# Kernel optimization log

Measured on AMD Instinct MI355X. Metric: run time of the kernel, lower is better.

The kernel has to match this reference:

```python
import jax, jax.numpy as jnp
import numpy as np

# ---- static config (matches init_kwargs) ----
B, L, D, H, NC = 2, 4096, 256, 8, 3
TOP_N, R = 8, 32              # top_n, vicinity_radius
LS, LE = 1000, 3000           # label_start, label_end
NL = 2                        # n_cross_attn_layers
FF = 4 * D                    # ffn_expand * d_model
Q_MAX = 2 * TOP_N * (2 * R + 1)  # 1040
HD = D // H


def setup_inputs() -> dict:
    key = jax.random.key(0)
    ks = jax.random.split(key, 12)
    def rn(k, shape, s=0.05):
        return jax.random.normal(k, shape, jnp.float32) * s
    return {
        "encoder_output": jax.random.normal(ks[0], (B, L, D), jnp.float32),
        "coarse_logits": jax.random.normal(ks[1], (B, L, NC), jnp.float32),
        "ln_q_g": jnp.ones((NL, D), jnp.float32),
        "ln_q_b": jnp.zeros((NL, D), jnp.float32),
        "ln_kv_g": jnp.ones((NL, D), jnp.float32),
        "ln_kv_b": jnp.zeros((NL, D), jnp.float32),
        "Wq": rn(ks[2], (NL, D, D)), "bq": jnp.zeros((NL, D), jnp.float32),
        "Wk": rn(ks[3], (NL, D, D)), "bk": jnp.zeros((NL, D), jnp.float32),
        "Wv": rn(ks[4], (NL, D, D)), "bv": jnp.zeros((NL, D), jnp.float32),
        "Wo": rn(ks[5], (NL, D, D)), "bo": jnp.zeros((NL, D), jnp.float32),
        "ffn_g": jnp.ones((NL, D), jnp.float32),
        "ffn_b": jnp.zeros((NL, D), jnp.float32),
        "W1": rn(ks[6], (NL, D, FF)), "b1": jnp.zeros((NL, FF), jnp.float32),
        "W2": rn(ks[7], (NL, FF, D)), "b2": jnp.zeros((NL, D), jnp.float32),
        "head_W": rn(ks[8], (D, NC)), "head_b": jnp.zeros((NC,), jnp.float32),
    }


def _layer_norm(x, g, b, eps=1e-5):
    m = jnp.mean(x, axis=-1, keepdims=True)
    v = jnp.mean(jnp.square(x - m), axis=-1, keepdims=True)
    return (x - m) * jax.lax.rsqrt(v + eps) * g + b


def _select_vicinities(coarse_logits):
    # eval mode: no gumbel noise. Returns (vicinity_idx (B,Q_MAX) int32 with
    # sentinel L at pad/dup slots, q_pad_mask (B,Q_MAX) bool).
    lp = jax.nn.log_softmax(coarse_logits.astype(jnp.float32), axis=-1)
    pos = jnp.arange(L)
    region = (pos >= LS) & (pos < LE)
    acc = jnp.where(region, lp[..., 1], -jnp.inf)
    don = jnp.where(region, lp[..., 2], -jnp.inf)
    _, don_idx = jax.lax.top_k(don, TOP_N)
    _, acc_idx = jax.lax.top_k(acc, TOP_N)
    centers = jnp.concatenate([don_idx, acc_idx], axis=-1)        # (B, 2*TOP_N)
    offsets = jnp.arange(-R, R + 1)
    vic = jnp.clip(centers[:, :, None] + offsets, 0, L - 1).reshape(B, -1)
    s = jnp.sort(vic, axis=-1)
    is_first = jnp.concatenate(
        [jnp.ones((B, 1), bool), s[:, 1:] != s[:, :-1]], axis=-1)
    idx = jnp.where(is_first, s, L)  # sentinel L -> zero row of scratch
    return idx, is_first


def reference(encoder_output, coarse_logits, ln_q_g, ln_q_b, ln_kv_g, ln_kv_b,
              Wq, bq, Wk, bk, Wv, bv, Wo, bo, ffn_g, ffn_b, W1, b1, W2, b2,
              head_W, head_b):
    idx, mask = _select_vicinities(coarse_logits)      # torch.no_grad() region
    idx = jax.lax.stop_gradient(idx)
    mask = jax.lax.stop_gradient(mask)

    scratch = jnp.pad(encoder_output, ((0, 0), (0, 1), (0, 0)))   # (B, L+1, D)
    q_stream = jnp.take_along_axis(scratch, idx[:, :, None], axis=1)  # (B,Q,D)
    kv = encoder_output
    m3 = mask[:, :, None]

    for i in range(NL):
        q_in = _layer_norm(q_stream, ln_q_g[i], ln_q_b[i])
        kv_in = _layer_norm(kv, ln_kv_g[i], ln_kv_b[i])
        q = (q_in @ Wq[i] + bq[i]).reshape(B, Q_MAX, H, HD)
        k = (kv_in @ Wk[i] + bk[i]).reshape(B, L, H, HD)
        v = (kv_in @ Wv[i] + bv[i]).reshape(B, L, H, HD)
        scores = jnp.einsum('bqhd,bkhd->bhqk', q, k) / jnp.sqrt(
            jnp.float32(HD))
        attn = jax.nn.softmax(scores, axis=-1)
        ao = jnp.einsum('bhqk,bkhd->bqhd', attn, v).reshape(B, Q_MAX, D)
        q_stream = q_stream + ao @ Wo[i] + bo[i]
        q_stream = jnp.where(m3, q_stream, 0.0)
        h = _layer_norm(q_stream, ffn_g[i], ffn_b[i])
        h = jax.nn.gelu(h @ W1[i] + b1[i], approximate=False) @ W2[i] + b2[i]
        q_stream = jnp.where(m3, q_stream + h, 0.0)

    out_scratch = scratch.at[jnp.arange(B)[:, None], idx].set(q_stream)
    refined = out_scratch[:, :L]                                  # drop sentinel
    refined_logits = refined @ head_W + head_b                    # (B, L, 3)
    return refined_logits
```

## Files before the change

### kernel.cpp

```cpp
#include <hip/hip_runtime.h>
#include <cmath>

constexpr int B = 2, L = 4096, D = 256, H = 8, NC = 3;
constexpr int TOP_N = 8, R = 32;
constexpr int LS = 1000, LE = 3000;
constexpr int NL = 2;
constexpr int FF = 4 * D;
constexpr int Q_MAX = 2 * TOP_N * (2 * R + 1);
constexpr int HD = D / H;
constexpr int QROWS = B * Q_MAX;
constexpr int KVROWS = B * L;
constexpr int NQT = (Q_MAX + 31) / 32;
constexpr int NREG = LE - LS;
constexpr int NSPLIT = 8;
constexpr int KCHUNK = L / NSPLIT;
constexpr int NT = KCHUNK / 32;
constexpr int KVBLK = 8 * (KVROWS / 64);
constexpr int QBLK = 4 * ((QROWS + 63) / 64);

typedef __attribute__((ext_vector_type(8))) short bf16x8;
typedef __attribute__((ext_vector_type(4))) float f32x4;
typedef __attribute__((ext_vector_type(4))) int i32x4;
typedef unsigned short u16;

union fr {
  bf16x8 h;
  i32x4 i;
};

__device__ __forceinline__ u16 f2bs(float f) {
  unsigned int u = __float_as_uint(f);
  unsigned int r = u + 0x7fffu + ((u >> 16) & 1u);
  return (u16)(r >> 16);
}
__device__ __forceinline__ float bs2f(u16 s) {
  return __uint_as_float(((unsigned int)s) << 16);
}
__device__ __forceinline__ float gelu_exact(float x) {
  return 0.5f * x * (1.f + erff(x * 0.70710678118654752440f));
}
__device__ __forceinline__ unsigned cvt_pk(float lo, float hi) {
  unsigned r;
  asm("v_cvt_pk_bf16_f32 %0, %1, %2" : "=v"(r) : "v"(lo), "v"(hi));
  return r;
}

#define GLL16(gsrc, ldst)                                                   \
  __builtin_amdgcn_global_load_lds(                                         \
      (const __attribute__((address_space(1))) unsigned int*)(gsrc),        \
      (__attribute__((address_space(3))) unsigned int*)(ldst), 16, 0, 0)

__global__ __launch_bounds__(1024) void select_kernel(
    const float* __restrict__ logits, int* __restrict__ idx_out,
    int* __restrict__ mask_out) {
  int b = blockIdx.x;
  int tid = threadIdx.x;
  int w = tid >> 6, lane = tid & 63;
  __shared__ float candv[16][8];
  __shared__ int candi[16][8];
  __shared__ int centers[2 * TOP_N];
  __shared__ unsigned present[L / 32];
  __shared__ int offs[128];
  __shared__ int wtot[2];

  float vd[2], va[2];
  int pidx[2];
#pragma unroll
  for (int j = 0; j < 2; ++j) {
    int p = tid + j * 1024;
    pidx[j] = p;
    if (p < NREG) {
      const float* lg = logits + ((long)b * L + LS + p) * NC;
      float x0 = lg[0], x1 = lg[1], x2 = lg[2];
      float m = fmaxf(x0, fmaxf(x1, x2));
      float lse = m + logf(expf(x0 - m) + expf(x1 - m) + expf(x2 - m));
      vd[j] = x2 - lse;
      va[j] = x1 - lse;
    } else {
      vd[j] = -INFINITY;
      va[j] = -INFINITY;
    }
  }
  if (tid < 128) present[tid] = 0;

  for (int sel = 0; sel < 2; ++sel) {
    float v0 = (sel == 0) ? vd[0] : va[0];
    float v1 = (sel == 0) ? vd[1] : va[1];
#pragma unroll
    for (int r = 0; r < TOP_N; ++r) {
      float mv;
      int mi;
      if (v0 >= v1) { mv = v0; mi = pidx[0]; }
      else { mv = v1; mi = pidx[1]; }
#pragma unroll
      for (int off = 32; off; off >>= 1) {
        float ov = __shfl_xor(mv, off, 64);
        int oi = __shfl_xor(mi, off, 64);
        if (ov > mv || (ov == mv && oi < mi)) { mv = ov; mi = oi; }
      }
      if (pidx[0] == mi) v0 = -INFINITY;
      if (pidx[1] == mi) v1 = -INFINITY;
      if (lane == 0) { candv[w][r] = mv; candi[w][r] = mi; }
    }
    __syncthreads();
    if (tid < 64) {
      int j0 = tid, j1 = tid + 64;
      float c0 = candv[j0 >> 3][j0 & 7], c1 = candv[j1 >> 3][j1 & 7];
      int i0 = candi[j0 >> 3][j0 & 7], i1 = candi[j1 >> 3][j1 & 7];
#pragma unroll
      for (int r = 0; r < TOP_N; ++r) {
        float mv;
        int mi;
        if (c0 > c1 || (c0 == c1 && i0 < i1)) { mv = c0; mi = i0; }
        else { mv = c1; mi = i1; }
#pragma unroll
        for (int off = 32; off; off >>= 1) {
          float ov = __shfl_xor(mv, off, 64);
          int oi = __shfl_xor(mi, off, 64);
          if (ov > mv || (ov == mv && oi < mi)) { mv = ov; mi = oi; }
        }
        if (i0 == mi) c0 = -INFINITY;
        if (i1 == mi) c1 = -INFINITY;
        if (tid == 0) centers[sel * TOP_N + r] = LS + mi;
      }
    }
    __syncthreads();
  }

  for (int j = tid; j < Q_MAX; j += 1024) {
    int c = centers[j / (2 * R + 1)];
    int off = j % (2 * R + 1) - R;
    int v = c + off;
    v = v < 0 ? 0 : (v > L - 1 ? L - 1 : v);
    atomicOr(&present[v >> 5], 1u << (v & 31));
  }
  __syncthreads();

  int cnt = (tid < 128) ? __popc(present[tid]) : 0;
  if (tid < 128) {
    int x = cnt;
#pragma unroll
    for (int off = 1; off < 64; off <<= 1) {
      int o = __shfl_up(x, off, 64);
      if ((tid & 63) >= off) x += o;
    }
    if ((tid & 63) == 63) wtot[tid >> 6] = x;
    offs[tid] = x - cnt;
  }
  __syncthreads();
  int total = wtot[0] + wtot[1];
  if (tid < 128) {
    int base = offs[tid] + ((tid >= 64) ? wtot[0] : 0);
    unsigned mword = present[tid];
    while (mword) {
      int i = __ffs(mword) - 1;
      mword &= mword - 1;
      idx_out[b * Q_MAX + base] = tid * 32 + i;
      mask_out[b * Q_MAX + base] = 1;
      ++base;
    }
  }
  for (int j = total + tid; j < Q_MAX; j += 1024) {
    idx_out[b * Q_MAX + j] = L;
    mask_out[b * Q_MAX + j] = 0;
  }
}

__global__ __launch_bounds__(256) void gather_kernel(
    const float* __restrict__ enc, const int* __restrict__ idx,
    float* __restrict__ q_stream) {
  int row = blockIdx.x;
  int b = row / Q_MAX;
  int p = idx[row];
  float v = 0.f;
  if (p < L) v = enc[((long)b * L + p) * D + threadIdx.x];
  q_stream[(long)row * D + threadIdx.x] = v;
}

__global__ __launch_bounds__(256) void ln_bf16(
    const float* __restrict__ in, u16* __restrict__ out,
    const float* __restrict__ gg, const float* __restrict__ bb) {
  long row = blockIdx.x;
  int tid = threadIdx.x;
  float x = in[row * D + tid];
  float s1 = x, s2 = x * x;
#pragma unroll
  for (int off = 32; off; off >>= 1) {
    s1 += __shfl_xor(s1, off, 64);
    s2 += __shfl_xor(s2, off, 64);
  }
  __shared__ float p1[4], p2[4];
  int w = tid >> 6;
  if ((tid & 63) == 0) { p1[w] = s1; p2[w] = s2; }
  __syncthreads();
  s1 = p1[0] + p1[1] + p1[2] + p1[3];
  s2 = p2[0] + p2[1] + p2[2] + p2[3];
  float mean = s1 * (1.f / D);
  float var = fmaxf(s2 * (1.f / D) - mean * mean, 0.f);
  float r = rsqrtf(var + 1e-5f);
  out[row * D + tid] = f2bs((x - mean) * r * gg[tid] + bb[tid]);
}

__global__ __launch_bounds__(256) void ln_kv2(
    const float* __restrict__ in, u16* __restrict__ o0, u16* __restrict__ o1,
    const float* __restrict__ gg, const float* __restrict__ bb) {
  long row = blockIdx.x;
  int tid = threadIdx.x;
  float x = in[row * D + tid];
  float s1 = x, s2 = x * x;
#pragma unroll
  for (int off = 32; off; off >>= 1) {
    s1 += __shfl_xor(s1, off, 64);
    s2 += __shfl_xor(s2, off, 64);
  }
  __shared__ float p1[4], p2[4];
  int w = tid >> 6;
  if ((tid & 63) == 0) { p1[w] = s1; p2[w] = s2; }
  __syncthreads();
  s1 = p1[0] + p1[1] + p1[2] + p1[3];
  s2 = p2[0] + p2[1] + p2[2] + p2[3];
  float mean = s1 * (1.f / D);
  float var = fmaxf(s2 * (1.f / D) - mean * mean, 0.f);
  float r = rsqrtf(var + 1e-5f);
  float xn = (x - mean) * r;
  o0[row * D + tid] = f2bs(xn * gg[tid] + bb[tid]);
  o1[row * D + tid] = f2bs(xn * gg[D + tid] + bb[D + tid]);
}

__global__ __launch_bounds__(256) void transpose_tiled(
    const float* __restrict__ Wq_, const float* __restrict__ Wk_,
    const float* __restrict__ Wv_, const float* __restrict__ Wo_,
    const float* __restrict__ W1_, const float* __restrict__ W2_,
    u16* __restrict__ WT) {
  __shared__ u16 T[64][65];
  const long DD = (long)D * D, DFF = (long)D * FF;
  const long LSTR = 4 * DD + 2 * DFF;
  int t = blockIdx.x;
  int l = t / 192, r = t % 192;
  const float* src;
  long dbase;
  int K_, N_, kt, nt;
  if (r < 64) {
    int which = r >> 4, sub = r & 15;
    kt = sub >> 2;
    nt = sub & 3;
    K_ = 256;
    N_ = 256;
    src = (which == 0 ? Wk_ : which == 1 ? Wv_ : which == 2 ? Wq_ : Wo_) +
          (long)l * DD;
    dbase = (long)l * LSTR + (long)which * DD;
  } else if (r < 128) {
    int sub = r - 64;
    kt = sub >> 4;
    nt = sub & 15;
    K_ = 256;
    N_ = 1024;
    src = W1_ + (long)l * DFF;
    dbase = (long)l * LSTR + 4 * DD;
  } else {
    int sub = r - 128;
    kt = sub >> 2;
    nt = sub & 3;
    K_ = 1024;
    N_ = 256;
    src = W2_ + (long)l * DFF;
    dbase = (long)l * LSTR + 4 * DD + DFF;
  }
  int k0 = kt * 64, n0 = nt * 64;
  {
    int kr = threadIdx.x >> 2, c16 = (threadIdx.x & 3) * 16;
    const float* sp = src + (long)(k0 + kr) * N_ + n0 + c16;
#pragma unroll
    for (int i = 0; i < 4; ++i) {
      float4 v = *reinterpret_cast<const float4*>(sp + 4 * i);
      T[kr][c16 + 4 * i + 0] = f2bs(v.x);
      T[kr][c16 + 4 * i + 1] = f2bs(v.y);
      T[kr][c16 + 4 * i + 2] = f2bs(v.z);
      T[kr][c16 + 4 * i + 3] = f2bs(v.w);
    }
  }
  __syncthreads();
  {
    int nr = threadIdx.x >> 2, kc = (threadIdx.x & 3) * 16;
    u16 tmp[16];
#pragma unroll
    for (int j = 0; j < 16; ++j) tmp[j] = T[kc + j][nr];
    u16* dp = WT + dbase + (long)(n0 + nr) * K_ + k0 + kc;
    *reinterpret_cast<bf16x8*>(dp) = *reinterpret_cast<const bf16x8*>(&tmp[0]);
    *reinterpret_cast<bf16x8*>(dp + 8) =
        *reinterpret_cast<const bf16x8*>(&tmp[8]);
  }
}

template <int EPI>
__global__ __launch_bounds__(256) void gemm_mfma(
    const u16* __restrict__ A, const u16* __restrict__ BT,
    const float* __restrict__ bias, void* __restrict__ Cv,
    const float* __restrict__ resid, const int* __restrict__ mask, int M,
    int N, int K) {
  __shared__ short As[64][40];
  __shared__ short Bs[64][40];
  int bm = blockIdx.y * 64, bn = blockIdx.x * 64;
  int tid = threadIdx.x;
  int lane = tid & 63, w = tid >> 6;
  int g = lane >> 4, li = lane & 15;
  int wr = w >> 1, wc = w & 1;
  f32x4 acc[2][2] = {};

  int srow = tid >> 2, skc = (tid & 3) * 8;
  for (int k0 = 0; k0 < K; k0 += 32) {
    {
      int grow = bm + srow;
      bf16x8 av = {};
      if (grow < M)
        av = *reinterpret_cast<const bf16x8*>(A + (long)grow * K + k0 + skc);
      *reinterpret_cast<bf16x8*>(&As[srow][skc]) = av;
      bf16x8 bv = *reinterpret_cast<const bf16x8*>(
          BT + (long)(bn + srow) * K + k0 + skc);
      *reinterpret_cast<bf16x8*>(&Bs[srow][skc]) = bv;
    }
    __syncthreads();
    bf16x8 a0 = *reinterpret_cast<const bf16x8*>(&As[wr * 32 + li][g * 8]);
    bf16x8 a1 = *reinterpret_cast<const bf16x8*>(&As[wr * 32 + 16 + li][g * 8]);
    bf16x8 b0 = *reinterpret_cast<const bf16x8*>(&Bs[wc * 32 + li][g * 8]);
    bf16x8 b1 = *reinterpret_cast<const bf16x8*>(&Bs[wc * 32 + 16 + li][g * 8]);
    acc[0][0] = __builtin_amdgcn_mfma_f32_16x16x32_bf16(a0, b0, acc[0][0], 0, 0, 0);
    acc[0][1] = __builtin_amdgcn_mfma_f32_16x16x32_bf16(a0, b1, acc[0][1], 0, 0, 0);
    acc[1][0] = __builtin_amdgcn_mfma_f32_16x16x32_bf16(a1, b0, acc[1][0], 0, 0, 0);
    acc[1][1] = __builtin_amdgcn_mfma_f32_16x16x32_bf16(a1, b1, acc[1][1], 0, 0, 0);
    __syncthreads();
  }

#pragma unroll
  for (int mr = 0; mr < 2; ++mr)
#pragma unroll
    for (int nr = 0; nr < 2; ++nr)
#pragma unroll
      for (int r = 0; r < 4; ++r) {
        int row = bm + wr * 32 + mr * 16 + g * 4 + r;
        int col = bn + wc * 32 + nr * 16 + li;
        if (row >= M) continue;
        float v = acc[mr][nr][r] + bias[col];
        if (EPI == 1) v = gelu_exact(v);
        if (EPI == 2) {
          v += resid[(long)row * N + col];
          v = mask[row] ? v : 0.f;
          ((float*)Cv)[(long)row * N + col] = v;
        } else {
          ((u16*)Cv)[(long)row * N + col] = f2bs(v);
        }
      }
}

__global__ __launch_bounds__(256) void gemm_proj(
    const u16* __restrict__ Akv, const u16* __restrict__ Aq,
    const u16* __restrict__ WTbase, const float* __restrict__ biasK,
    const float* __restrict__ biasV, const float* __restrict__ biasQ,
    u16* __restrict__ Kh, u16* __restrict__ Vh, u16* __restrict__ Qb) {
  __shared__ short As[64][40];
  __shared__ short Bs[64][40];
  __shared__ u16 Ct[64][72];
  int bid = blockIdx.x;
  int tid = threadIdx.x;
  int lane = tid & 63, w = tid >> 6;
  int g = lane >> 4, li = lane & 15;
  int wr = w >> 1, wc = w & 1;
  f32x4 acc[2][2] = {};
  const long DD = (long)D * D;

  bool isKV = bid < KVBLK;
  int bm, bn, M;
  const u16* A;
  const u16* BT;
  if (isKV) {
    bn = (bid & 7) * 64;
    bm = (bid >> 3) * 64;
    M = KVROWS;
    A = Akv;
    BT = WTbase;
  } else {
    int qb = bid - KVBLK;
    bn = (qb & 3) * 64;
    bm = (qb >> 2) * 64;
    M = QROWS;
    A = Aq;
    BT = WTbase + 2 * DD;
  }

  int srow = tid >> 2, skc = (tid & 3) * 8;
  for (int k0 = 0; k0 < D; k0 += 32) {
    {
      int grow = bm + srow;
      bf16x8 av = {};
      if (grow < M)
        av = *reinterpret_cast<const bf16x8*>(A + (long)grow * D + k0 + skc);
      *reinterpret_cast<bf16x8*>(&As[srow][skc]) = av;
      bf16x8 bv = *reinterpret_cast<const bf16x8*>(
          BT + (long)(bn + srow) * D + k0 + skc);
      *reinterpret_cast<bf16x8*>(&Bs[srow][skc]) = bv;
    }
    __syncthreads();
    bf16x8 a0 = *reinterpret_cast<const bf16x8*>(&As[wr * 32 + li][g * 8]);
    bf16x8 a1 = *reinterpret_cast<const bf16x8*>(&As[wr * 32 + 16 + li][g * 8]);
    bf16x8 b0 = *reinterpret_cast<const bf16x8*>(&Bs[wc * 32 + li][g * 8]);
    bf16x8 b1 = *reinterpret_cast<const bf16x8*>(&Bs[wc * 32 + 16 + li][g * 8]);
    acc[0][0] = __builtin_amdgcn_mfma_f32_16x16x32_bf16(a0, b0, acc[0][0], 0, 0, 0);
    acc[0][1] = __builtin_amdgcn_mfma_f32_16x16x32_bf16(a0, b1, acc[0][1], 0, 0, 0);
    acc[1][0] = __builtin_amdgcn_mfma_f32_16x16x32_bf16(a1, b0, acc[1][0], 0, 0, 0);
    acc[1][1] = __builtin_amdgcn_mfma_f32_16x16x32_bf16(a1, b1, acc[1][1], 0, 0, 0);
    __syncthreads();
  }

  if (!isKV) {
#pragma unroll
    for (int mr = 0; mr < 2; ++mr)
#pragma unroll
      for (int nr = 0; nr < 2; ++nr)
#pragma unroll
        for (int r = 0; r < 4; ++r) {
          int row = bm + wr * 32 + mr * 16 + g * 4 + r;
          int col = bn + wc * 32 + nr * 16 + li;
          if (row >= M) continue;
          Qb[(long)row * D + col] = f2bs(acc[mr][nr][r] + biasQ[col]);
        }
  } else if (bn < 256) {
#pragma unroll
    for (int mr = 0; mr < 2; ++mr)
#pragma unroll
      for (int nr = 0; nr < 2; ++nr)
#pragma unroll
        for (int r = 0; r < 4; ++r) {
          int rowL = wr * 32 + mr * 16 + g * 4 + r;
          int colL = wc * 32 + nr * 16 + li;
          Ct[rowL][colL] = f2bs(acc[mr][nr][r] + biasK[bn + colL]);
        }
    __syncthreads();
#pragma unroll
    for (int p = 0; p < 2; ++p) {
      int rowL = (tid >> 3) + p * 32;
      int c8 = (tid & 7) * 8;
      int grow = bm + rowL;
      int b2 = grow >> 12, key = grow & (L - 1);
      int gcol = bn + c8;
      int hh = gcol >> 5, dd = gcol & (HD - 1);
      int cst = (dd >> 3) ^ ((key >> 1) & 3);
      u16* dst = Kh + (((long)(b2 * H + hh) * L + key) * 32 + (cst << 3));
      *reinterpret_cast<bf16x8*>(dst) =
          *reinterpret_cast<const bf16x8*>(&Ct[rowL][c8]);
    }
  } else {
    int vbn = bn - 256;
#pragma unroll
    for (int mr = 0; mr < 2; ++mr)
#pragma unroll
      for (int nr = 0; nr < 2; ++nr)
#pragma unroll
        for (int r = 0; r < 4; ++r) {
          int rowL = wr * 32 + mr * 16 + g * 4 + r;
          int colL = wc * 32 + nr * 16 + li;
          Ct[colL][rowL] = f2bs(acc[mr][nr][r] + biasV[vbn + colL]);
        }
    __syncthreads();
    int b2 = bm >> 12;
#pragma unroll
    for (int p = 0; p < 2; ++p) {
      int colL = (tid >> 3) + p * 32;
      int rem = tid & 7;
      int kb = rem >> 2, k8 = (rem & 3) * 8;
      int gcol = vbn + colL;
      int hh = gcol >> 5, dd = gcol & (HD - 1);
      int kb32 = ((bm & (L - 1)) >> 5) + kb;
      int j = (k8 >> 2) ^ ((dd >> 1) & 6);
      u16* dst = Vh + (((long)(b2 * H + hh) * (L / 32) + kb32) * 1024 +
                       dd * 32 + (j << 2));
      *reinterpret_cast<bf16x8*>(dst) =
          *reinterpret_cast<const bf16x8*>(&Ct[colL][kb * 32 + k8]);
    }
  }
}

constexpr int POOLSZ = NSPLIT * 32 * 33 * 4 + NSPLIT * 32 * 4;

__global__ __launch_bounds__(512) void attn_mfma(
    const u16* __restrict__ Qb, const u16* __restrict__ Kh,
    const u16* __restrict__ Vh, u16* __restrict__ AO) {
  __shared__ alignas(16) char pool[POOLSZ];
  int i = blockIdx.x;
  int xcd = i & 7, slot = i >> 3;
  int bh = (xcd << 1) | (slot >= NQT ? 1 : 0);
  int qt = (slot >= NQT) ? slot - NQT : slot;
  int h = bh & 7;
  int b = bh >> 3;
  int tid = threadIdx.x, w = tid >> 6, lane = tid & 63;
  int g = lane >> 4, li = lane & 15;

  fr qf0, qf1;
  {
    const float QSC = 0.25509836048f;
#pragma unroll
    for (int qb = 0; qb < 2; ++qb) {
      int qrow = qt * 32 + qb * 16 + li;
      if (qrow >= Q_MAX) qrow = Q_MAX - 1;
      bf16x8 raw = *reinterpret_cast<const bf16x8*>(
          Qb + ((long)(b * Q_MAX + qrow)) * D + h * HD + g * 8);
      fr& qf = qb ? qf1 : qf0;
#pragma unroll
      for (int j = 0; j < 4; ++j)
        qf.i[j] = (int)cvt_pk(bs2f((u16)raw[2 * j]) * QSC,
                              bs2f((u16)raw[2 * j + 1]) * QSC);
    }
  }

  f32x4 acc00 = {}, acc01 = {}, acc10 = {}, acc11 = {};
// ... 47 lines not shown
    for (int r = 0; r < 4; ++r) {
      p00[r] = exp2f(s00[r]);
      p10[r] = exp2f(s10[r]);
      p01[r] = exp2f(s01[r]);
      p11[r] = exp2f(s11[r]);
      den0 += p00[r] + p10[r];
      den1 += p01[r] + p11[r];
    }
    fr pf0, pf1;
    pf0.i[0] = (int)cvt_pk(p00[0], p00[1]);
    pf0.i[1] = (int)cvt_pk(p00[2], p00[3]);
    pf0.i[2] = (int)cvt_pk(p10[0], p10[1]);
    pf0.i[3] = (int)cvt_pk(p10[2], p10[3]);
    pf1.i[0] = (int)cvt_pk(p01[0], p01[1]);
    pf1.i[1] = (int)cvt_pk(p01[2], p01[3]);
    pf1.i[2] = (int)cvt_pk(p11[0], p11[1]);
    pf1.i[3] = (int)cvt_pk(p11[2], p11[3]);

    fr v0, v1;
    v0.i = (i32x4){(int)va0.x, (int)va0.y, (int)vb0.x, (int)vb0.y};
    v1.i = (i32x4){(int)va1.x, (int)va1.y, (int)vb1.x, (int)vb1.y};
    acc00 = __builtin_amdgcn_mfma_f32_16x16x32_bf16(v0.h, pf0.h, acc00, 0, 0, 0);
    acc01 = __builtin_amdgcn_mfma_f32_16x16x32_bf16(v0.h, pf1.h, acc01, 0, 0, 0);
    acc10 = __builtin_amdgcn_mfma_f32_16x16x32_bf16(v1.h, pf0.h, acc10, 0, 0, 0);
    acc11 = __builtin_amdgcn_mfma_f32_16x16x32_bf16(v1.h, pf1.h, acc11, 0, 0, 0);
  }

  den0 += __shfl_xor(den0, 16, 64);
  den0 += __shfl_xor(den0, 32, 64);
  den1 += __shfl_xor(den1, 16, 64);
  den1 += __shfl_xor(den1, 32, 64);

  __syncthreads();
  float (*accs)[32][33] = (float(*)[32][33])pool;
  float (*dsh)[32] = (float(*)[32])(pool + NSPLIT * 32 * 33 * 4);
#pragma unroll
  for (int r = 0; r < 4; ++r) {
    accs[w][g * 4 + r][li] = acc00[r];
    accs[w][g * 4 + r][16 + li] = acc01[r];
    accs[w][16 + g * 4 + r][li] = acc10[r];
    accs[w][16 + g * 4 + r][16 + li] = acc11[r];
  }
  if (g == 0) {
    dsh[w][li] = den0;
    dsh[w][16 + li] = den1;
  }
  __syncthreads();

  int q = tid >> 4, dp = tid & 15;
  float Den = 0.f, o0 = 0.f, o1 = 0.f;
#pragma unroll
  for (int ww = 0; ww < NSPLIT; ++ww) {
    Den += dsh[ww][q];
    o0 += accs[ww][2 * dp][q];
    o1 += accs[ww][2 * dp + 1][q];
  }
  float inv = 1.f / Den;
  int qrow = qt * 32 + q;
  if (qrow < Q_MAX) {
    unsigned pk = cvt_pk(o0 * inv, o1 * inv);
    *reinterpret_cast<unsigned*>(
        AO + ((long)(b * Q_MAX + qrow)) * D + h * HD + 2 * dp) = pk;
  }
}

__global__ __launch_bounds__(256) void head_kernel(
    const float* __restrict__ enc, const float* __restrict__ hW,
    const float* __restrict__ hb, float* __restrict__ out) {
// ... 45 lines not shown
extern "C" void kernel_launch(void* const* d_in, const int* in_sizes, int n_in,
                              void* d_out, int out_size, void* d_ws,
                              size_t ws_size, hipStream_t stream) {
  const float* enc = (const float*)d_in[0];
  const float* clog = (const float*)d_in[1];
  const float* ln_q_g = (const float*)d_in[2];
  const float* ln_q_b = (const float*)d_in[3];
  const float* ln_kv_g = (const float*)d_in[4];
  const float* ln_kv_b = (const float*)d_in[5];
  const float* Wq = (const float*)d_in[6];
  const float* bq = (const float*)d_in[7];
  const float* Wk = (const float*)d_in[8];
  const float* bk = (const float*)d_in[9];
  const float* Wv = (const float*)d_in[10];
  const float* bv = (const float*)d_in[11];
  const float* Wo = (const float*)d_in[12];
  const float* bo = (const float*)d_in[13];
  const float* ffn_g = (const float*)d_in[14];
  const float* ffn_b = (const float*)d_in[15];
  const float* W1 = (const float*)d_in[16];
  const float* b1 = (const float*)d_in[17];
  const float* W2 = (const float*)d_in[18];
  const float* b2 = (const float*)d_in[19];
  const float* head_W = (const float*)d_in[20];
  const float* head_b = (const float*)d_in[21];
  float* out = (float*)d_out;

  char* ws = (char*)d_ws;
  float* q_stream = (float*)ws;            ws += (long)QROWS * D * 4;
  u16* kvl0 = (u16*)ws;                    ws += (long)KVROWS * D * 2;
  u16* kvl1 = (u16*)ws;                    ws += (long)KVROWS * D * 2;
  u16* Khbuf = (u16*)ws;                   ws += (long)B * H * L * HD * 2;
  u16* Vhbuf = (u16*)ws;                   ws += (long)B * H * L * HD * 2;
  u16* q_ln = (u16*)ws;                    ws += (long)QROWS * D * 2;
  u16* Qbuf = (u16*)ws;                    ws += (long)QROWS * D * 2;
  u16* AObuf = (u16*)ws;                   ws += (long)QROWS * D * 2;
  u16* H1buf = (u16*)ws;                   ws += (long)QROWS * FF * 2;
  u16* WT = (u16*)ws;                      ws += (long)NL * (4 * D * D + 2 * D * FF) * 2;
  int* idxbuf = (int*)ws;                  ws += QROWS * 4;
  int* maskbuf = (int*)ws;

  const long DD = (long)D * D, DFF = (long)D * FF;
  const long LSTR = 4 * DD + 2 * DFF;

  transpose_tiled<<<NL * 192, 256, 0, stream>>>(Wq, Wk, Wv, Wo, W1, W2, WT);
  ln_kv2<<<KVROWS, 256, 0, stream>>>(enc, kvl0, kvl1, ln_kv_g, ln_kv_b);
  select_kernel<<<B, 1024, 0, stream>>>(clog, idxbuf, maskbuf);
  gather_kernel<<<QROWS, 256, 0, stream>>>(enc, idxbuf, q_stream);

  for (int l = 0; l < NL; ++l) {
    u16* base = WT + l * LSTR;
    u16* kv_ln = (l == 0) ? kvl0 : kvl1;

    ln_bf16<<<QROWS, 256, 0, stream>>>(q_stream, q_ln, ln_q_g + l * D, ln_q_b + l * D);

    gemm_proj<<<KVBLK + QBLK, 256, 0, stream>>>(
        kv_ln, q_ln, base, bk + l * D, bv + l * D, bq + l * D, Khbuf, Vhbuf,
        Qbuf);

    attn_mfma<<<B * H * NQT, 512, 0, stream>>>(Qbuf, Khbuf, Vhbuf, AObuf);

    dim3 gQ(D / 64, (QROWS + 63) / 64);
    gemm_mfma<2><<<gQ, 256, 0, stream>>>(AObuf, base + 3 * DD, bo + l * D,
                                         (void*)q_stream, q_stream, maskbuf,
                                         QROWS, D, D);

    ln_bf16<<<QROWS, 256, 0, stream>>>(q_stream, q_ln, ffn_g + l * D, ffn_b + l * D);
    dim3 gF1(FF / 64, (QROWS + 63) / 64);
    gemm_mfma<1><<<gF1, 256, 0, stream>>>(q_ln, base + 4 * DD, b1 + l * FF,
                                          (void*)H1buf, nullptr, nullptr,
                                          QROWS, FF, D);
    dim3 gF2(D / 64, (QROWS + 63) / 64);
    gemm_mfma<2><<<gF2, 256, 0, stream>>>(H1buf, base + 4 * DD + DFF,
                                          b2 + l * D, (void*)q_stream,
                                          q_stream, maskbuf, QROWS, D, FF);
  }

  head_kernel<<<KVROWS / 4, 256, 0, stream>>>(enc, head_W, head_b, out);
  overwrite_kernel<<<QROWS, 64, 0, stream>>>(q_stream, idxbuf, maskbuf, head_W,
                                             head_b, out);
}
```

Before: 230.5 us.

## Fuse setup kernels and fold query/FFN layernorms into GEMM prologues

Merges the weight transpose, KV layernorm and vicinity selection into one setup kernel, and reworks selection to use 256 threads. Removes the standalone ln_bf16 launches by computing the layernorm inside the Q projection and FFN1 GEMMs, with a full 64x256 normalized A tile staged in shared memory. This cuts kernel launches and intermediate bf16 round trips. The cost is fewer, longer-running blocks for the Q and FFN1 GEMMs, which may lower parallelism.

```diff
diff --git a/kernel.cpp b/kernel.cpp
--- a/kernel.cpp
+++ b/kernel.cpp
@@ -16,7 +16,8 @@
 constexpr int KCHUNK = L / NSPLIT;
 constexpr int NT = KCHUNK / 32;
 constexpr int KVBLK = 8 * (KVROWS / 64);
-constexpr int QBLK = 4 * ((QROWS + 63) / 64);
+constexpr int QRB = (QROWS + 63) / 64;
+constexpr int TRBLK = NL * 192;
 
 typedef __attribute__((ext_vector_type(8))) short bf16x8;
 typedef __attribute__((ext_vector_type(4))) float f32x4;
@@ -50,119 +51,213 @@
       (const __attribute__((address_space(1))) unsigned int*)(gsrc),        \
       (__attribute__((address_space(3))) unsigned int*)(ldst), 16, 0, 0)
 
-__global__ __launch_bounds__(1024) void select_kernel(
-    const float* __restrict__ logits, int* __restrict__ idx_out,
-    int* __restrict__ mask_out) {
-  int b = blockIdx.x;
+__global__ __launch_bounds__(256) void setup_kernel(
+    const float* __restrict__ enc, const float* __restrict__ logits,
+    const float* __restrict__ lnkvg, const float* __restrict__ lnkvb,
+    const float* __restrict__ Wq_, const float* __restrict__ Wk_,
+    const float* __restrict__ Wv_, const float* __restrict__ Wo_,
+    const float* __restrict__ W1_, const float* __restrict__ W2_,
+    u16* __restrict__ WT, u16* __restrict__ o0, u16* __restrict__ o1,
+    int* __restrict__ idx_out, int* __restrict__ mask_out) {
+  int bid = blockIdx.x;
   int tid = threadIdx.x;
-  int w = tid >> 6, lane = tid & 63;
-  __shared__ float candv[16][8];
-  __shared__ int candi[16][8];
-  __shared__ int centers[2 * TOP_N];
-  __shared__ unsigned present[L / 32];
-  __shared__ int offs[128];
-  __shared__ int wtot[2];
-
-  float vd[2], va[2];
-  int pidx[2];
-#pragma unroll
-  for (int j = 0; j < 2; ++j) {
-    int p = tid + j * 1024;
-    pidx[j] = p;
-    if (p < NREG) {
-      const float* lg = logits + ((long)b * L + LS + p) * NC;
-      float x0 = lg[0], x1 = lg[1], x2 = lg[2];
-      float m = fmaxf(x0, fmaxf(x1, x2));
-      float lse = m + logf(expf(x0 - m) + expf(x1 - m) + expf(x2 - m));
-      vd[j] = x2 - lse;
-      va[j] = x1 - lse;
+  const long DD = (long)D * D, DFF = (long)D * FF;
+  const long LSTR = 4 * DD + 2 * DFF;
+
+  if (bid < KVROWS) {
+    long row = bid;
+    float x = enc[row * D + tid];
+    float s1 = x, s2 = x * x;
+#pragma unroll
+    for (int off = 32; off; off >>= 1) {
+      s1 += __shfl_xor(s1, off, 64);
+      s2 += __shfl_xor(s2, off, 64);
+    }
+    __shared__ float p1[4], p2[4];
+    int w = tid >> 6;
+    if ((tid & 63) == 0) { p1[w] = s1; p2[w] = s2; }
+    __syncthreads();
+    s1 = p1[0] + p1[1] + p1[2] + p1[3];
+    s2 = p2[0] + p2[1] + p2[2] + p2[3];
+    float mean = s1 * (1.f / D);
+    float var = fmaxf(s2 * (1.f / D) - mean * mean, 0.f);
+    float r = rsqrtf(var + 1e-5f);
+    float xn = (x - mean) * r;
+    o0[row * D + tid] = f2bs(xn * lnkvg[tid] + lnkvb[tid]);
+    o1[row * D + tid] = f2bs(xn * lnkvg[D + tid] + lnkvb[D + tid]);
+    return;
+  }
+
+  if (bid < KVROWS + TRBLK) {
+    __shared__ u16 T[64][65];
+    int t = bid - KVROWS;
+    int l = t / 192, r = t % 192;
+    const float* src;
+    long dbase;
+    int K_, N_, kt, nt;
+    if (r < 64) {
+      int which = r >> 4, sub = r & 15;
+      kt = sub >> 2;
+      nt = sub & 3;
+      K_ = 256;
+      N_ = 256;
+      src = (which == 0 ? Wk_ : which == 1 ? Wv_ : which == 2 ? Wq_ : Wo_) +
+            (long)l * DD;
+      dbase = (long)l * LSTR + (long)which * DD;
+    } else if (r < 128) {
+      int sub = r - 64;
+      kt = sub >> 4;
+      nt = sub & 15;
+      K_ = 256;
+      N_ = 1024;
+      src = W1_ + (long)l * DFF;
+      dbase = (long)l * LSTR + 4 * DD;
     } else {
-      vd[j] = -INFINITY;
-      va[j] = -INFINITY;
-    }
-  }
-  if (tid < 128) present[tid] = 0;
-
-  for (int sel = 0; sel < 2; ++sel) {
-    float v0 = (sel == 0) ? vd[0] : va[0];
-    float v1 = (sel == 0) ? vd[1] : va[1];
-#pragma unroll
-    for (int r = 0; r < TOP_N; ++r) {
-      float mv;
-      int mi;
-      if (v0 >= v1) { mv = v0; mi = pidx[0]; }
-      else { mv = v1; mi = pidx[1]; }
-#pragma unroll
-      for (int off = 32; off; off >>= 1) {
-        float ov = __shfl_xor(mv, off, 64);
-        int oi = __shfl_xor(mi, off, 64);
-        if (ov > mv || (ov == mv && oi < mi)) { mv = ov; mi = oi; }
+      int sub = r - 128;
+      kt = sub >> 2;
+      nt = sub & 3;
+      K_ = 1024;
+      N_ = 256;
+      src = W2_ + (long)l * DFF;
+      dbase = (long)l * LSTR + 4 * DD + DFF;
+    }
+    int k0 = kt * 64, n0 = nt * 64;
+    {
+      int kr = tid >> 2, c16 = (tid & 3) * 16;
+      const float* sp = src + (long)(k0 + kr) * N_ + n0 + c16;
+#pragma unroll
+      for (int i = 0; i < 4; ++i) {
+        float4 v = *reinterpret_cast<const float4*>(sp + 4 * i);
+        T[kr][c16 + 4 * i + 0] = f2bs(v.x);
+        T[kr][c16 + 4 * i + 1] = f2bs(v.y);
+        T[kr][c16 + 4 * i + 2] = f2bs(v.z);
+        T[kr][c16 + 4 * i + 3] = f2bs(v.w);
       }
-      if (pidx[0] == mi) v0 = -INFINITY;
-      if (pidx[1] == mi) v1 = -INFINITY;
-      if (lane == 0) { candv[w][r] = mv; candi[w][r] = mi; }
-    }
-    __syncthreads();
-    if (tid < 64) {
-      int j0 = tid, j1 = tid + 64;
-      float c0 = candv[j0 >> 3][j0 & 7], c1 = candv[j1 >> 3][j1 & 7];
-      int i0 = candi[j0 >> 3][j0 & 7], i1 = candi[j1 >> 3][j1 & 7];
+    }
+    __syncthreads();
+    {
+      int nr = tid >> 2, kc = (tid & 3) * 16;
+      u16 tmp[16];
+#pragma unroll
+      for (int j = 0; j < 16; ++j) tmp[j] = T[kc + j][nr];
+      u16* dp = WT + dbase + (long)(n0 + nr) * K_ + k0 + kc;
+      *reinterpret_cast<bf16x8*>(dp) = *reinterpret_cast<const bf16x8*>(&tmp[0]);
+      *reinterpret_cast<bf16x8*>(dp + 8) =
+          *reinterpret_cast<const bf16x8*>(&tmp[8]);
+    }
+    return;
+  }
+
+  {
+    int b = bid - KVROWS - TRBLK;
+    int w = tid >> 6, lane = tid & 63;
+    __shared__ float candv[4][8];
+    __shared__ int candi[4][8];
+    __shared__ int centers[2 * TOP_N];
+    __shared__ unsigned present[L / 32];
+    __shared__ int offs[128];
+    __shared__ int wtot[2];
+
+    float vd[8], va[8];
+#pragma unroll
+    for (int j = 0; j < 8; ++j) {
+      int p = tid + j * 256;
+      if (p < NREG) {
+        const float* lg = logits + ((long)b * L + LS + p) * NC;
+        float x0 = lg[0], x1 = lg[1], x2 = lg[2];
+        float m = fmaxf(x0, fmaxf(x1, x2));
+        float lse = m + logf(expf(x0 - m) + expf(x1 - m) + expf(x2 - m));
+        vd[j] = x2 - lse;
+        va[j] = x1 - lse;
+      } else {
+        vd[j] = -INFINITY;
+        va[j] = -INFINITY;
+      }
+    }
+    if (tid < 128) present[tid] = 0;
+
+    for (int sel = 0; sel < 2; ++sel) {
+      float v[8];
+#pragma unroll
+      for (int j = 0; j < 8; ++j) v[j] = (sel == 0) ? vd[j] : va[j];
 #pragma unroll
       for (int r = 0; r < TOP_N; ++r) {
-        float mv;
-        int mi;
-        if (c0 > c1 || (c0 == c1 && i0 < i1)) { mv = c0; mi = i0; }
-        else { mv = c1; mi = i1; }
+        float mv = v[0];
+        int mp = tid;
+#pragma unroll
+        for (int j = 1; j < 8; ++j) {
+          int pj = tid + j * 256;
+          if (v[j] > mv) { mv = v[j]; mp = pj; }
+        }
 #pragma unroll
         for (int off = 32; off; off >>= 1) {
           float ov = __shfl_xor(mv, off, 64);
-          int oi = __shfl_xor(mi, off, 64);
-          if (ov > mv || (ov == mv && oi < mi)) { mv = ov; mi = oi; }
+          int oi = __shfl_xor(mp, off, 64);
+          if (ov > mv || (ov == mv && oi < mp)) { mv = ov; mp = oi; }
         }
-        if (i0 == mi) c0 = -INFINITY;
-        if (i1 == mi) c1 = -INFINITY;
-        if (tid == 0) centers[sel * TOP_N + r] = LS + mi;
+#pragma unroll
+        for (int j = 0; j < 8; ++j)
+          if (tid + j * 256 == mp) v[j] = -INFINITY;
+        if (lane == 0) { candv[w][r] = mv; candi[w][r] = mp; }
       }
-    }
-    __syncthreads();
-  }
-
-  for (int j = tid; j < Q_MAX; j += 1024) {
-    int c = centers[j / (2 * R + 1)];
-    int off = j % (2 * R + 1) - R;
-    int v = c + off;
-    v = v < 0 ? 0 : (v > L - 1 ? L - 1 : v);
-    atomicOr(&present[v >> 5], 1u << (v & 31));
-  }
-  __syncthreads();
-
-  int cnt = (tid < 128) ? __popc(present[tid]) : 0;
-  if (tid < 128) {
-    int x = cnt;
-#pragma unroll
-    for (int off = 1; off < 64; off <<= 1) {
-      int o = __shfl_up(x, off, 64);
-      if ((tid & 63) >= off) x += o;
-    }
-    if ((tid & 63) == 63) wtot[tid >> 6] = x;
-    offs[tid] = x - cnt;
-  }
-  __syncthreads();
-  int total = wtot[0] + wtot[1];
-  if (tid < 128) {
-    int base = offs[tid] + ((tid >= 64) ? wtot[0] : 0);
-    unsigned mword = present[tid];
-    while (mword) {
-      int i = __ffs(mword) - 1;
-      mword &= mword - 1;
-      idx_out[b * Q_MAX + base] = tid * 32 + i;
-      mask_out[b * Q_MAX + base] = 1;
-      ++base;
-    }
-  }
-  for (int j = total + tid; j < Q_MAX; j += 1024) {
-    idx_out[b * Q_MAX + j] = L;
-    mask_out[b * Q_MAX + j] = 0;
+      __syncthreads();
+      if (tid < 64) {
+        float c = (tid < 32) ? candv[tid >> 3][tid & 7] : -INFINITY;
+        int ci = (tid < 32) ? candi[tid >> 3][tid & 7] : 0x7fffffff;
+#pragma unroll
+        for (int r = 0; r < TOP_N; ++r) {
+          float mv = c;
+          int mi = ci;
+#pragma unroll
+          for (int off = 32; off; off >>= 1) {
+            float ov = __shfl_xor(mv, off, 64);
+            int oi = __shfl_xor(mi, off, 64);
+            if (ov > mv || (ov == mv && oi < mi)) { mv = ov; mi = oi; }
+          }
+          if (ci == mi) c = -INFINITY;
+          if (tid == 0) centers[sel * TOP_N + r] = LS + mi;
+        }
+      }
+      __syncthreads();
+    }
+
+    for (int j = tid; j < Q_MAX; j += 256) {
+      int c = centers[j / (2 * R + 1)];
+      int off = j % (2 * R + 1) - R;
+      int v2 = c + off;
+      v2 = v2 < 0 ? 0 : (v2 > L - 1 ? L - 1 : v2);
+      atomicOr(&present[v2 >> 5], 1u << (v2 & 31));
+    }
+    __syncthreads();
+
+    int cnt = (tid < 128) ? __popc(present[tid]) : 0;
+    if (tid < 128) {
+      int x = cnt;
+#pragma unroll
+      for (int off = 1; off < 64; off <<= 1) {
+        int o = __shfl_up(x, off, 64);
+        if ((tid & 63) >= off) x += o;
+      }
+      if ((tid & 63) == 63) wtot[tid >> 6] = x;
+      offs[tid] = x - cnt;
+    }
+    __syncthreads();
+    int total = wtot[0] + wtot[1];
+    if (tid < 128) {
+      int base = offs[tid] + ((tid >= 64) ? wtot[0] : 0);
+      unsigned mword = present[tid];
+      while (mword) {
+        int i = __ffs(mword) - 1;
+        mword &= mword - 1;
+        idx_out[b * Q_MAX + base] = tid * 32 + i;
+        mask_out[b * Q_MAX + base] = 1;
+        ++base;
+      }
+    }
+    for (int j = total + tid; j < Q_MAX; j += 256) {
+      idx_out[b * Q_MAX + j] = L;
+      mask_out[b * Q_MAX + j] = 0;
+    }
   }
 }
 
@@ -177,118 +272,46 @@
   q_stream[(long)row * D + threadIdx.x] = v;
 }
 
-__global__ __launch_bounds__(256) void ln_bf16(
-    const float* __restrict__ in, u16* __restrict__ out,
-    const float* __restrict__ gg, const float* __restrict__ bb) {
-  long row = blockIdx.x;
-  int tid = threadIdx.x;
-  float x = in[row * D + tid];
-  float s1 = x, s2 = x * x;
-#pragma unroll
-  for (int off = 32; off; off >>= 1) {
-    s1 += __shfl_xor(s1, off, 64);
-    s2 += __shfl_xor(s2, off, 64);
-  }
-  __shared__ float p1[4], p2[4];
-  int w = tid >> 6;
-  if ((tid & 63) == 0) { p1[w] = s1; p2[w] = s2; }
-  __syncthreads();
-  s1 = p1[0] + p1[1] + p1[2] + p1[3];
-  s2 = p2[0] + p2[1] + p2[2] + p2[3];
-  float mean = s1 * (1.f / D);
-  float var = fmaxf(s2 * (1.f / D) - mean * mean, 0.f);
-  float r = rsqrtf(var + 1e-5f);
-  out[row * D + tid] = f2bs((x - mean) * r * gg[tid] + bb[tid]);
-}
-
-__global__ __launch_bounds__(256) void ln_kv2(
-    const float* __restrict__ in, u16* __restrict__ o0, u16* __restrict__ o1,
-    const float* __restrict__ gg, const float* __restrict__ bb) {
-  long row = blockIdx.x;
-  int tid = threadIdx.x;
-  float x = in[row * D + tid];
-  float s1 = x, s2 = x * x;
-#pragma unroll
-  for (int off = 32; off; off >>= 1) {
-    s1 += __shfl_xor(s1, off, 64);
-    s2 += __shfl_xor(s2, off, 64);
-  }
-  __shared__ float p1[4], p2[4];
-  int w = tid >> 6;
-  if ((tid & 63) == 0) { p1[w] = s1; p2[w] = s2; }
-  __syncthreads();
-  s1 = p1[0] + p1[1] + p1[2] + p1[3];
-  s2 = p2[0] + p2[1] + p2[2] + p2[3];
-  float mean = s1 * (1.f / D);
-  float var = fmaxf(s2 * (1.f / D) - mean * mean, 0.f);
-  float r = rsqrtf(var + 1e-5f);
-  float xn = (x - mean) * r;
-  o0[row * D + tid] = f2bs(xn * gg[tid] + bb[tid]);
-  o1[row * D + tid] = f2bs(xn * gg[D + tid] + bb[D + tid]);
-}
-
-__global__ __launch_bounds__(256) void transpose_tiled(
-    const float* __restrict__ Wq_, const float* __restrict__ Wk_,
-    const float* __restrict__ Wv_, const float* __restrict__ Wo_,
-    const float* __restrict__ W1_, const float* __restrict__ W2_,
-    u16* __restrict__ WT) {
-  __shared__ u16 T[64][65];
-  const long DD = (long)D * D, DFF = (long)D * FF;
-  const long LSTR = 4 * DD + 2 * DFF;
-  int t = blockIdx.x;
-  int l = t / 192, r = t % 192;
-  const float* src;
-  long dbase;
-  int K_, N_, kt, nt;
-  if (r < 64) {
-    int which = r >> 4, sub = r & 15;
-    kt = sub >> 2;
-    nt = sub & 3;
-    K_ = 256;
-    N_ = 256;
-    src = (which == 0 ? Wk_ : which == 1 ? Wv_ : which == 2 ? Wq_ : Wo_) +
-          (long)l * DD;
-    dbase = (long)l * LSTR + (long)which * DD;
-  } else if (r < 128) {
-    int sub = r - 64;
-    kt = sub >> 4;
-    nt = sub & 15;
-    K_ = 256;
-    N_ = 1024;
-    src = W1_ + (long)l * DFF;
-    dbase = (long)l * LSTR + 4 * DD;
-  } else {
-    int sub = r - 128;
-    kt = sub >> 2;
-    nt = sub & 3;
-    K_ = 1024;
-    N_ = 256;
-    src = W2_ + (long)l * DFF;
-    dbase = (long)l * LSTR + 4 * DD + DFF;
-  }
-  int k0 = kt * 64, n0 = nt * 64;
-  {
-    int kr = threadIdx.x >> 2, c16 = (threadIdx.x & 3) * 16;
-    const float* sp = src + (long)(k0 + kr) * N_ + n0 + c16;
-#pragma unroll
-    for (int i = 0; i < 4; ++i) {
-      float4 v = *reinterpret_cast<const float4*>(sp + 4 * i);
-      T[kr][c16 + 4 * i + 0] = f2bs(v.x);
-      T[kr][c16 + 4 * i + 1] = f2bs(v.y);
-      T[kr][c16 + 4 * i + 2] = f2bs(v.z);
-      T[kr][c16 + 4 * i + 3] = f2bs(v.w);
-    }
-  }
-  __syncthreads();
-  {
-    int nr = threadIdx.x >> 2, kc = (threadIdx.x & 3) * 16;
-    u16 tmp[16];
-#pragma unroll
-    for (int j = 0; j < 16; ++j) tmp[j] = T[kc + j][nr];
-    u16* dp = WT + dbase + (long)(n0 + nr) * K_ + k0 + kc;
-    *reinterpret_cast<bf16x8*>(dp) = *reinterpret_cast<const bf16x8*>(&tmp[0]);
-    *reinterpret_cast<bf16x8*>(dp + 8) =
-        *reinterpret_cast<const bf16x8*>(&tmp[8]);
+__device__ __forceinline__ void ln_stage(
+    const float* __restrict__ A, int bm, int M, const float* __restrict__ lng,
+    const float* __restrict__ lnb, u16 (*As)[264], int tid) {
+  int r = tid >> 2, qd = tid & 3;
+  int grow = bm + r;
+  if (grow >= M) grow = M - 1;
+  const float* ap = A + ((long)grow) * D + qd * 64;
+  float sum = 0.f, ss = 0.f;
+#pragma unroll
+  for (int i = 0; i < 16; ++i) {
+    float4 v = *reinterpret_cast<const float4*>(ap + i * 4);
+    sum += v.x + v.y + v.z + v.w;
+    ss += v.x * v.x + v.y * v.y + v.z * v.z + v.w * v.w;
+  }
+  sum += __shfl_xor(sum, 1, 64);
+  sum += __shfl_xor(sum, 2, 64);
+  ss += __shfl_xor(ss, 1, 64);
+  ss += __shfl_xor(ss, 2, 64);
+  float mean = sum * (1.f / D);
+  float var = fmaxf(ss * (1.f / D) - mean * mean, 0.f);
+  float rstd = rsqrtf(var + 1e-5f);
+#pragma unroll
+  for (int i = 0; i < 8; ++i) {
+    int k = qd * 64 + i * 8;
+    float4 xa = *reinterpret_cast<const float4*>(ap + i * 8);
+    float4 xb = *reinterpret_cast<const float4*>(ap + i * 8 + 4);
+    float4 ga = *reinterpret_cast<const float4*>(lng + k);
+    float4 gb = *reinterpret_cast<const float4*>(lng + k + 4);
+    float4 ba = *reinterpret_cast<const float4*>(lnb + k);
+    float4 bb = *reinterpret_cast<const float4*>(lnb + k + 4);
+    fr v;
+    v.i[0] = (int)cvt_pk((xa.x - mean) * rstd * ga.x + ba.x,
+                         (xa.y - mean) * rstd * ga.y + ba.y);
+    v.i[1] = (int)cvt_pk((xa.z - mean) * rstd * ga.z + ba.z,
+                         (xa.w - mean) * rstd * ga.w + ba.w);
+    v.i[2] = (int)cvt_pk((xb.x - mean) * rstd * gb.x + bb.x,
+                         (xb.y - mean) * rstd * gb.y + bb.y);
+    v.i[3] = (int)cvt_pk((xb.z - mean) * rstd * gb.z + bb.z,
+                         (xb.w - mean) * rstd * gb.w + bb.w);
+    *reinterpret_cast<bf16x8*>(&As[r][k]) = v.h;
   }
 }
 
@@ -353,50 +376,75 @@
 }
 
 __global__ __launch_bounds__(256) void gemm_proj(
-    const u16* __restrict__ Akv, const u16* __restrict__ Aq,
-    const u16* __restrict__ WTbase, const float* __restrict__ biasK,
+    const u16* __restrict__ Akv, const float* __restrict__ Aqf,
+    const u16* __restrict__ WTbase, const float* __restrict__ lnqg,
+    const float* __restrict__ lnqb, const float* __restrict__ biasK,
     const float* __restrict__ biasV, const float* __restrict__ biasQ,
     u16* __restrict__ Kh, u16* __restrict__ Vh, u16* __restrict__ Qb) {
-  __shared__ short As[64][40];
-  __shared__ short Bs[64][40];
-  __shared__ u16 Ct[64][72];
+  __shared__ alignas(16) char pool[64 * 264 * 2 + 64 * 40 * 2];
   int bid = blockIdx.x;
   int tid = threadIdx.x;
   int lane = tid & 63, w = tid >> 6;
   int g = lane >> 4, li = lane & 15;
   int wr = w >> 1, wc = w & 1;
+  const long DD = (long)D * D;
+
+  if (bid >= KVBLK) {
+    u16(*As)[264] = (u16(*)[264])pool;
+    u16(*Bs)[40] = (u16(*)[40])(pool + 64 * 264 * 2);
+    int bm = (bid - KVBLK) * 64;
+    ln_stage(Aqf, bm, QROWS, lnqg, lnqb, As, tid);
+    __syncthreads();
+    const u16* BT = WTbase + 2 * DD;
+    int srow = tid >> 2, skc = (tid & 3) * 8;
+    for (int nt = 0; nt < 4; ++nt) {
+      int bn = nt * 64;
+      f32x4 acc[2][2] = {};
+      for (int k0 = 0; k0 < D; k0 += 32) {
+        *reinterpret_cast<bf16x8*>(&Bs[srow][skc]) =
+            *reinterpret_cast<const bf16x8*>(BT + (long)(bn + srow) * D + k0 + skc);
+        __syncthreads();
+        bf16x8 a0 = *reinterpret_cast<const bf16x8*>(&As[wr * 32 + li][k0 + g * 8]);
+        bf16x8 a1 =
+            *reinterpret_cast<const bf16x8*>(&As[wr * 32 + 16 + li][k0 + g * 8]);
+        bf16x8 b0 = *reinterpret_cast<const bf16x8*>(&Bs[wc * 32 + li][g * 8]);
+        bf16x8 b1 = *reinterpret_cast<const bf16x8*>(&Bs[wc * 32 + 16 + li][g * 8]);
+        acc[0][0] = __builtin_amdgcn_mfma_f32_16x16x32_bf16(a0, b0, acc[0][0], 0, 0, 0);
+        acc[0][1] = __builtin_amdgcn_mfma_f32_16x16x32_bf16(a0, b1, acc[0][1], 0, 0, 0);
+        acc[1][0] = __builtin_amdgcn_mfma_f32_16x16x32_bf16(a1, b0, acc[1][0], 0, 0, 0);
+        acc[1][1] = __builtin_amdgcn_mfma_f32_16x16x32_bf16(a1, b1, acc[1][1], 0, 0, 0);
+        __syncthreads();
+      }
+#pragma unroll
+      for (int mr = 0; mr < 2; ++mr)
+#pragma unroll
+        for (int nr = 0; nr < 2; ++nr)
+#pragma unroll
+          for (int r = 0; r < 4; ++r) {
+            int row = bm + wr * 32 + mr * 16 + g * 4 + r;
+            int col = bn + wc * 32 + nr * 16 + li;
+            if (row >= QROWS) continue;
+            Qb[(long)row * D + col] = f2bs(acc[mr][nr][r] + biasQ[col]);
+          }
+    }
+    return;
+  }
+
+  short(*As)[40] = (short(*)[40])pool;
+  short(*Bs)[40] = (short(*)[40])(pool + 64 * 40 * 2);
+  u16(*Ct)[72] = (u16(*)[72])(pool + 2 * 64 * 40 * 2);
+  int bn = (bid & 7) * 64;
+  int bm = (bid >> 3) * 64;
   f32x4 acc[2][2] = {};
-  const long DD = (long)D * D;
-
-  bool isKV = bid < KVBLK;
-  int bm, bn, M;
-  const u16* A;
-  const u16* BT;
-  if (isKV) {
-    bn = (bid & 7) * 64;
-    bm = (bid >> 3) * 64;
-    M = KVROWS;
-    A = Akv;
-    BT = WTbase;
-  } else {
-    int qb = bid - KVBLK;
-    bn = (qb & 3) * 64;
-    bm = (qb >> 2) * 64;
-    M = QROWS;
-    A = Aq;
-    BT = WTbase + 2 * DD;
-  }
 
   int srow = tid >> 2, skc = (tid & 3) * 8;
   for (int k0 = 0; k0 < D; k0 += 32) {
     {
-      int grow = bm + srow;
-      bf16x8 av = {};
-      if (grow < M)
-        av = *reinterpret_cast<const bf16x8*>(A + (long)grow * D + k0 + skc);
+      bf16x8 av = *reinterpret_cast<const bf16x8*>(
+          Akv + (long)(bm + srow) * D + k0 + skc);
       *reinterpret_cast<bf16x8*>(&As[srow][skc]) = av;
       bf16x8 bv = *reinterpret_cast<const bf16x8*>(
-          BT + (long)(bn + srow) * D + k0 + skc);
+          WTbase + (long)(bn + srow) * D + k0 + skc);
       *reinterpret_cast<bf16x8*>(&Bs[srow][skc]) = bv;
     }
     __syncthreads();
@@ -411,19 +459,7 @@
     __syncthreads();
   }
 
-  if (!isKV) {
-#pragma unroll
-    for (int mr = 0; mr < 2; ++mr)
-#pragma unroll
-      for (int nr = 0; nr < 2; ++nr)
-#pragma unroll
-        for (int r = 0; r < 4; ++r) {
-          int row = bm + wr * 32 + mr * 16 + g * 4 + r;
-          int col = bn + wc * 32 + nr * 16 + li;
-          if (row >= M) continue;
-          Qb[(long)row * D + col] = f2bs(acc[mr][nr][r] + biasQ[col]);
-        }
-  } else if (bn < 256) {
+  if (bn < 256) {
 #pragma unroll
     for (int mr = 0; mr < 2; ++mr)
 #pragma unroll
@@ -479,6 +515,55 @@
   }
 }
 
+__global__ __launch_bounds__(256) void gemm_ffn1(
+    const float* __restrict__ A, const u16* __restrict__ BT,
+    const float* __restrict__ lng, const float* __restrict__ lnb,
+    const float* __restrict__ bias, u16* __restrict__ H1) {
+  __shared__ alignas(16) char pool[64 * 264 * 2 + 64 * 40 * 2];
+  u16(*As)[264] = (u16(*)[264])pool;
+  u16(*Bs)[40] = (u16(*)[40])(pool + 64 * 264 * 2);
+  int tid = threadIdx.x;
+  int lane = tid & 63, w = tid >> 6;
+  int g = lane >> 4, li = lane & 15;
+  int wr = w >> 1, wc = w & 1;
+  int bm = blockIdx.y * 64;
+
+  ln_stage(A, bm, QROWS, lng, lnb, As, tid);
+  __syncthreads();
+
+  int srow = tid >> 2, skc = (tid & 3) * 8;
+  for (int nt = 0; nt < 4; ++nt) {
+    int bn = blockIdx.x * 256 + nt * 64;
+    f32x4 acc[2][2] = {};
+    for (int k0 = 0; k0 < D; k0 += 32) {
+      *reinterpret_cast<bf16x8*>(&Bs[srow][skc]) =
+          *reinterpret_cast<const bf16x8*>(BT + (long)(bn + srow) * D + k0 + skc);
+      __syncthreads();
+      bf16x8 a0 = *reinterpret_cast<const bf16x8*>(&As[wr * 32 + li][k0 + g * 8]);
+      bf16x8 a1 =
+          *reinterpret_cast<const bf16x8*>(&As[wr * 32 + 16 + li][k0 + g * 8]);
+      bf16x8 b0 = *reinterpret_cast<const bf16x8*>(&Bs[wc * 32 + li][g * 8]);
+      bf16x8 b1 = *reinterpret_cast<const bf16x8*>(&Bs[wc * 32 + 16 + li][g * 8]);
+      acc[0][0] = __builtin_amdgcn_mfma_f32_16x16x32_bf16(a0, b0, acc[0][0], 0, 0, 0);
+      acc[0][1] = __builtin_amdgcn_mfma_f32_16x16x32_bf16(a0, b1, acc[0][1], 0, 0, 0);
+      acc[1][0] = __builtin_amdgcn_mfma_f32_16x16x32_bf16(a1, b0, acc[1][0], 0, 0, 0);
+      acc[1][1] = __builtin_amdgcn_mfma_f32_16x16x32_bf16(a1, b1, acc[1][1], 0, 0, 0);
+      __syncthreads();
+    }
+#pragma unroll
+    for (int mr = 0; mr < 2; ++mr)
+#pragma unroll
+      for (int nr = 0; nr < 2; ++nr)
+#pragma unroll
+        for (int r = 0; r < 4; ++r) {
+          int row = bm + wr * 32 + mr * 16 + g * 4 + r;
+          int col = bn + wc * 32 + nr * 16 + li;
+          if (row >= QROWS) continue;
+          H1[(long)row * FF + col] = f2bs(gelu_exact(acc[mr][nr][r] + bias[col]));
+        }
+  }
+}
+
 constexpr int POOLSZ = NSPLIT * 32 * 33 * 4 + NSPLIT * 32 * 4;
 
 __global__ __launch_bounds__(512) void attn_mfma(
@@ -592,8 +677,8 @@
   den1 += __shfl_xor(den1, 32, 64);
 
   __syncthreads();
-  float (*accs)[32][33] = (float(*)[32][33])pool;
-  float (*dsh)[32] = (float(*)[32])(pool + NSPLIT * 32 * 33 * 4);
+  float(*accs)[32][33] = (float(*)[32][33])pool;
+  float(*dsh)[32] = (float(*)[32])(pool + NSPLIT * 32 * 33 * 4);
 #pragma unroll
   for (int r = 0; r < 4; ++r) {
     accs[w][g * 4 + r][li] = acc00[r];
@@ -705,7 +790,6 @@
   u16* kvl1 = (u16*)ws;                    ws += (long)KVROWS * D * 2;
   u16* Khbuf = (u16*)ws;                   ws += (long)B * H * L * HD * 2;
   u16* Vhbuf = (u16*)ws;                   ws += (long)B * H * L * HD * 2;
-  u16* q_ln = (u16*)ws;                    ws += (long)QROWS * D * 2;
   u16* Qbuf = (u16*)ws;                    ws += (long)QROWS * D * 2;
   u16* AObuf = (u16*)ws;                   ws += (long)QROWS * D * 2;
   u16* H1buf = (u16*)ws;                   ws += (long)QROWS * FF * 2;
@@ -716,20 +800,18 @@
   const long DD = (long)D * D, DFF = (long)D * FF;
   const long LSTR = 4 * DD + 2 * DFF;
 
-  transpose_tiled<<<NL * 192, 256, 0, stream>>>(Wq, Wk, Wv, Wo, W1, W2, WT);
-  ln_kv2<<<KVROWS, 256, 0, stream>>>(enc, kvl0, kvl1, ln_kv_g, ln_kv_b);
-  select_kernel<<<B, 1024, 0, stream>>>(clog, idxbuf, maskbuf);
+  setup_kernel<<<KVROWS + TRBLK + B, 256, 0, stream>>>(
+      enc, clog, ln_kv_g, ln_kv_b, Wq, Wk, Wv, Wo, W1, W2, WT, kvl0, kvl1,
+      idxbuf, maskbuf);
   gather_kernel<<<QROWS, 256, 0, stream>>>(enc, idxbuf, q_stream);
 
   for (int l = 0; l < NL; ++l) {
     u16* base = WT + l * LSTR;
     u16* kv_ln = (l == 0) ? kvl0 : kvl1;
 
-    ln_bf16<<<QROWS, 256, 0, stream>>>(q_stream, q_ln, ln_q_g + l * D, ln_q_b + l * D);
-
-    gemm_proj<<<KVBLK + QBLK, 256, 0, stream>>>(
-        kv_ln, q_ln, base, bk + l * D, bv + l * D, bq + l * D, Khbuf, Vhbuf,
-        Qbuf);
+    gemm_proj<<<KVBLK + QRB, 256, 0, stream>>>(
+        kv_ln, q_stream, base, ln_q_g + l * D, ln_q_b + l * D, bk + l * D,
+        bv + l * D, bq + l * D, Khbuf, Vhbuf, Qbuf);
 
     attn_mfma<<<B * H * NQT, 512, 0, stream>>>(Qbuf, Khbuf, Vhbuf, AObuf);
 
@@ -738,11 +820,10 @@
                                          (void*)q_stream, q_stream, maskbuf,
                                          QROWS, D, D);
 
-    ln_bf16<<<QROWS, 256, 0, stream>>>(q_stream, q_ln, ffn_g + l * D, ffn_b + l * D);
-    dim3 gF1(FF / 64, (QROWS + 63) / 64);
-    gemm_mfma<1><<<gF1, 256, 0, stream>>>(q_ln, base + 4 * DD, b1 + l * FF,
-                                          (void*)H1buf, nullptr, nullptr,
-                                          QROWS, FF, D);
+    gemm_ffn1<<<dim3(4, QRB), 256, 0, stream>>>(
+        q_stream, base + 4 * DD, ffn_g + l * D, ffn_b + l * D, b1 + l * FF,
+        H1buf);
+
     dim3 gF2(D / 64, (QROWS + 63) / 64);
     gemm_mfma<2><<<gF2, 256, 0, stream>>>(H1buf, base + 4 * DD + DFF,
                                           b2 + l * D, (void*)q_stream,
```

Result: slower. 289.5 us (+25.6%).
